# Optimization experiments

Hardware: AMD Instinct MI355X
Metric: run time of the kernel (lower is better)

## Reference

```python
import jax, jax.numpy as jnp
import numpy as np

# Config (matches init_kwargs)
HQ, HKV, HD, WIN = 16, 4, 128, 512  # query heads, kv heads, head_dim, sliding window


def setup_inputs() -> dict:
    key = jax.random.key(0)
    k0, k1, k2, k3, k4 = jax.random.split(key, 5)
    B, S, D = 1, 8192, 2048
    std = 0.02
    hidden_states = jax.random.normal(k0, (B, S, D), jnp.float32)
    Wq = jax.random.normal(k1, (D, HQ * HD), jnp.float32) * std
    Wk = jax.random.normal(k2, (D, HKV * HD), jnp.float32) * std
    Wv = jax.random.normal(k3, (D, HKV * HD), jnp.float32) * std
    Wo = jax.random.normal(k4, (HQ * HD, D), jnp.float32) * std
    return {"hidden_states": hidden_states, "Wq": Wq, "Wk": Wk, "Wv": Wv, "Wo": Wo}


def _sliding_window_attention(q, k, v, win):
    # block i attend to keys of blocks i-1 and i -> scores [B,H,nb,W,2W].
    B, H, S, hd = q.shape
    W = win
    nb = S // W
    qb = q.reshape(B, H, nb, W, hd)
    kpad = jnp.pad(k, ((0, 0), (0, 0), (W, 0), (0, 0)))
    vpad = jnp.pad(v, ((0, 0), (0, 0), (W, 0), (0, 0)))
    kb = jnp.concatenate([kpad[:, :, :S].reshape(B, H, nb, W, hd),
                          k.reshape(B, H, nb, W, hd)], axis=3)  # [B,H,nb,2W,hd]
    vb = jnp.concatenate([vpad[:, :, :S].reshape(B, H, nb, W, hd),
                          v.reshape(B, H, nb, W, hd)], axis=3)
    # Faithful double-scaling of the source: /sqrt(hd) inside the chunk matmul
    # and again before softmax -> effective /hd.
    scores = jnp.einsum('bhnqd,bhnkd->bhnqk', qb, kb) / jnp.asarray(hd, qb.dtype)
    qi = jnp.arange(W)[:, None]
    ki = jnp.arange(2 * W)[None, :]
    # key local index k maps to global offset (k - W) relative to block start;
    # attend iff 0 <= q_glob - k_glob <= W-1  <=>  q+1 <= k <= q+W
    band = (ki >= qi + 1) & (ki <= qi + W)          # [W, 2W]
    blk = jnp.arange(nb)[:, None, None]
    valid = band[None] & ((blk > 0) | (ki[None] >= W))  # block 0 has no prev keys
    neg = jnp.finfo(scores.dtype).min
    scores = jnp.where(valid[None, None], scores, neg)
    probs = jax.nn.softmax(scores, axis=-1)
    out = jnp.einsum('bhnqk,bhnkd->bhnqd', probs, vb)
    return out.reshape(B, H, S, hd)


def reference(hidden_states, Wq, Wk, Wv, Wo):
    B, S, D = hidden_states.shape
    q = (hidden_states @ Wq).reshape(B, S, HQ, HD).transpose(0, 2, 1, 3)
    k = (hidden_states @ Wk).reshape(B, S, HKV, HD).transpose(0, 2, 1, 3)
    v = (hidden_states @ Wv).reshape(B, S, HKV, HD).transpose(0, 2, 1, 3)
    rep = HQ // HKV
    k = jnp.repeat(k, rep, axis=1)
    v = jnp.repeat(v, rep, axis=1)
    attn = _sliding_window_attention(q, k, v, WIN)      # [B,HQ,S,HD]
    attn = attn.transpose(0, 2, 1, 3).reshape(B, S, HQ * HD)
    return attn @ Wo
```

## Files before the change

kernel.cpp:

```cpp
#include <hip/hip_runtime.h>


typedef __bf16 bf16x8 __attribute__((ext_vector_type(8)));
typedef float f32x4 __attribute__((ext_vector_type(4)));
typedef int v8i __attribute__((ext_vector_type(8)));

__device__ __forceinline__ unsigned short f2bf(float f) {
  unsigned int u = __float_as_uint(f);
  u += 0x7fffu + ((u >> 16) & 1u);
  return (unsigned short)(u >> 16);
}

__device__ __forceinline__ f32x4 mfma16(bf16x8 a, bf16x8 b, f32x4 c) {
  return __builtin_amdgcn_mfma_f32_16x16x32_bf16(a, b, c, 0, 0, 0);
}

__device__ __forceinline__ void async16(void* lds, const void* g) {
  __builtin_amdgcn_global_load_lds(
      (__attribute__((address_space(1))) unsigned int*)g,
      (__attribute__((address_space(3))) unsigned int*)lds, 16, 0, 0);
}


__global__ __launch_bounds__(256) void convert_h_kernel(
    const float* __restrict__ src, unsigned short* __restrict__ dbf,
    unsigned char* __restrict__ d8, int n) {
  int i = (blockIdx.x * 256 + threadIdx.x) * 4;
  if (i < n) {
    float4 f = *(const float4*)(src + i);
    ushort4 o;
    o.x = f2bf(f.x); o.y = f2bf(f.y); o.z = f2bf(f.z); o.w = f2bf(f.w);
    *(ushort4*)(dbf + i) = o;
    int p = __builtin_amdgcn_cvt_pk_fp8_f32(f.x, f.y, 0, 0);
    p = __builtin_amdgcn_cvt_pk_fp8_f32(f.z, f.w, p, 1);
    *(unsigned int*)(d8 + i) = p;
  }
}

__global__ __launch_bounds__(256) void transpose_convert_kernel(
    const float* __restrict__ src, unsigned short* __restrict__ dst,
    int K, int N) {
  __shared__ unsigned short T[64 * 72];
  int kb = blockIdx.y * 64, nb = blockIdx.x * 64;
  int t = threadIdx.x;
  for (int u = t; u < 1024; u += 256) {
    int r = u >> 4, s = u & 15;
    float4 f = *(const float4*)(src + (size_t)(kb + r) * N + nb + s * 4);
    ushort4 o;
    o.x = f2bf(f.x); o.y = f2bf(f.y); o.z = f2bf(f.z); o.w = f2bf(f.w);
    *(ushort4*)&T[r * 72 + s * 4] = o;
  }
  __syncthreads();
  for (int u = t; u < 1024; u += 256) {
    int orow = u >> 4, s = u & 15;
    ushort4 o;
    o.x = T[(s * 4 + 0) * 72 + orow];
    o.y = T[(s * 4 + 1) * 72 + orow];
    o.z = T[(s * 4 + 2) * 72 + orow];
    o.w = T[(s * 4 + 3) * 72 + orow];
    *(ushort4*)(dst + (size_t)(nb + orow) * K + kb + s * 4) = o;
  }
}

__global__ __launch_bounds__(256) void transpose_convert_fp8_kernel(
    const float* __restrict__ src, unsigned char* __restrict__ dst,
    int K, int N) {
  __shared__ unsigned short T[64 * 72];
  int kb = blockIdx.y * 64, nb = blockIdx.x * 64;
  int t = threadIdx.x;
  for (int u = t; u < 1024; u += 256) {
    int r = u >> 4, s = u & 15;
    float4 f = *(const float4*)(src + (size_t)(kb + r) * N + nb + s * 4);
    ushort4 o;
    o.x = f2bf(f.x); o.y = f2bf(f.y); o.z = f2bf(f.z); o.w = f2bf(f.w);
    *(ushort4*)&T[r * 72 + s * 4] = o;
  }
  __syncthreads();
  for (int u = t; u < 1024; u += 256) {
    int orow = u >> 4, s = u & 15;
    float f0 = __uint_as_float((unsigned int)T[(s * 4 + 0) * 72 + orow] << 16);
    float f1 = __uint_as_float((unsigned int)T[(s * 4 + 1) * 72 + orow] << 16);
    float f2 = __uint_as_float((unsigned int)T[(s * 4 + 2) * 72 + orow] << 16);
    float f3 = __uint_as_float((unsigned int)T[(s * 4 + 3) * 72 + orow] << 16);
    int p = __builtin_amdgcn_cvt_pk_fp8_f32(f0, f1, 0, 0);
    p = __builtin_amdgcn_cvt_pk_fp8_f32(f2, f3, p, 1);
    *(unsigned int*)&dst[(size_t)(nb + orow) * K + kb + s * 4] = p;
  }
}

__global__ __launch_bounds__(256) void vtrans_kernel(
    const unsigned short* __restrict__ QKV, unsigned short* __restrict__ VTg) {
  int flat = blockIdx.x * 256 + threadIdx.x;
  int c = flat & 511;
  int s0 = (flat >> 9) * 8;
  unsigned short tmp[8];
  #pragma unroll
  for (int j = 0; j < 8; ++j)
    tmp[j] = QKV[(size_t)(s0 + j) * 3072 + 2560 + c];
  *(uint4*)&VTg[(size_t)c * 8192 + s0] = *(uint4*)tmp;
}


template <bool F32OUT>
__global__ __launch_bounds__(256) void gemm_bt_kernel(
    const unsigned short* __restrict__ A, const unsigned short* __restrict__ BT,
    void* __restrict__ Cp, int M, int ldc, int K) {
  __shared__ unsigned short As[128 * 32];
  __shared__ unsigned short Bs[128 * 32];
  int mb = blockIdx.y * 128, nb = blockIdx.x * 128;
  int tid = threadIdx.x;
  int lane = tid & 63, wv = tid >> 6;
  int wrow = wv >> 1, wcol = wv & 1;
  int lr = lane >> 2, ls = lane & 3;
  int fr = lane & 15, fg = lane >> 4;
  f32x4 acc[4][4] = {};
  for (int k0 = 0; k0 < K; k0 += 32) {
    __syncthreads();
    #pragma unroll
    for (int r = 0; r < 2; ++r) {
      int s = wv * 2 + r;
      async16(&As[s * 512], &A[(size_t)(mb + s * 16 + lr) * K + k0 + ls * 8]);
      async16(&Bs[s * 512], &BT[(size_t)(nb + s * 16 + lr) * K + k0 + ls * 8]);
    }
    __syncthreads();
    bf16x8 a[4], b[4];
    #pragma unroll
    for (int rt = 0; rt < 4; ++rt)
      a[rt] = *(const bf16x8*)&As[(wrow * 64 + rt * 16 + fr) * 32 + fg * 8];
    #pragma unroll
    for (int ct = 0; ct < 4; ++ct)
      b[ct] = *(const bf16x8*)&Bs[(wcol * 64 + ct * 16 + fr) * 32 + fg * 8];
    #pragma unroll
    for (int rt = 0; rt < 4; ++rt)
      #pragma unroll
      for (int ct = 0; ct < 4; ++ct)
        acc[rt][ct] = mfma16(a[rt], b[ct], acc[rt][ct]);
  }
  #pragma unroll
  for (int rt = 0; rt < 4; ++rt)
    #pragma unroll
    for (int ct = 0; ct < 4; ++ct)
      #pragma unroll
      for (int i = 0; i < 4; ++i) {
        int row = mb + wrow * 64 + rt * 16 + fg * 4 + i;
        int col = nb + wcol * 64 + ct * 16 + fr;
        if constexpr (F32OUT)
          ((float*)Cp)[(size_t)row * ldc + col] = acc[rt][ct][i];
        else
          ((unsigned short*)Cp)[(size_t)row * ldc + col] = f2bf(acc[rt][ct][i]);
      }
}


__global__ __launch_bounds__(512, 2) void gemm8p_oproj_kernel(
    const unsigned short* __restrict__ A, const unsigned short* __restrict__ BT,
    float* __restrict__ C, int ldc, int K) {
  __shared__ unsigned char lds[131072];
  const int mb = blockIdx.y * 256, nb = blockIdx.x * 256;
  const int tid = threadIdx.x;
  const int lane = tid & 63, wv = tid >> 6;
  const int wm = wv >> 2, wn = wv & 3;
  const int fr = lane & 15, fg = lane >> 4;
  const int xr = (fr & 4) ? 32 : 0;
  const int a_base = (wm * 128 + fr) * 128 + ((fg * 16) ^ xr);
  const int b_base = (wn * 64 + fr) * 128 + ((fg * 16) ^ xr);
  const int lsw = (lane * 16) ^ (lane & 32);
  const int lrow = lsw >> 7, lcol = (lsw & 127) >> 1;
  const int NT = K >> 6;

  f32x4 acc[8][4] = {};
  bf16x8 aF[4][2], bF[2][2];

#define FENCE_ asm volatile("" ::: "memory")
#define BAR_ { FENCE_; __builtin_amdgcn_s_barrier(); FENCE_; }
#define LGKM0_ asm volatile("s_waitcnt lgkmcnt(0)" ::: "memory")
#define STAGE_A_(BUFI, T, HALF)                                              \
  { _Pragma("unroll")                                                        \
    for (int l = 0; l < 2; ++l) {                                            \
      int cc = wv * 2 + l;                                                   \
      int rb = (cc >> 3) * 128 + (HALF) * 64 + (cc & 7) * 8;                 \
      async16(lds + (BUFI) * 65536 + rb * 128,                               \
              A + (size_t)(mb + rb + lrow) * K + (T) * 64 + lcol);           \
    } }
#define STAGE_B_(BUFI, T, HALF)                                              \
  { _Pragma("unroll")                                                        \
    for (int l = 0; l < 2; ++l) {                                            \
      int cc = wv * 2 + l;                                                   \
      int rb = (cc >> 2) * 64 + (HALF) * 32 + (cc & 3) * 8;                  \
      async16(lds + (BUFI) * 65536 + 32768 + rb * 128,                       \
              BT + (size_t)(nb + rb + lrow) * K + (T) * 64 + lcol);          \
    } }
#define LOAD_A_(HALF)                                                        \
  { _Pragma("unroll")                                                        \
    for (int q = 0; q < 4; ++q)                                              \
      _Pragma("unroll")                                                      \
      for (int kk = 0; kk < 2; ++kk)                                         \
        aF[q][kk] =                                                          \
            *(const bf16x8*)&Ab_[a_base + ((HALF)*4 + q) * 2048 + kk * 64]; }
#define LOAD_B_(HALF)                                                        \
  { _Pragma("unroll")                                                        \
    for (int c2 = 0; c2 < 2; ++c2)                                           \
      _Pragma("unroll")                                                      \
      for (int kk = 0; kk < 2; ++kk)                                         \
        bF[c2][kk] =                                                         \
            *(const bf16x8*)&Bb_[b_base + ((HALF)*2 + c2) * 2048 + kk * 64]; }
#define MFMA_(RT0, CT0)                                                      \
  { __builtin_amdgcn_s_setprio(1);                                           \
    _Pragma("unroll")                                                        \
    for (int q = 0; q < 4; ++q)                                              \
      _Pragma("unroll")                                                      \
      for (int c2 = 0; c2 < 2; ++c2) {                                       \
        acc[(RT0) + q][(CT0) + c2] =                                         \
            mfma16(aF[q][0], bF[c2][0], acc[(RT0) + q][(CT0) + c2]);         \
        acc[(RT0) + q][(CT0) + c2] =                                         \
            mfma16(aF[q][1], bF[c2][1], acc[(RT0) + q][(CT0) + c2]);         \
      }                                                                      \
    __builtin_amdgcn_s_setprio(0); }

  STAGE_A_(0, 0, 0); STAGE_A_(0, 0, 1); STAGE_B_(0, 0, 0); STAGE_B_(0, 0, 1);
  STAGE_B_(1, 1, 0); STAGE_A_(1, 1, 1);
  asm volatile("s_waitcnt vmcnt(4)" ::: "memory");
  BAR_;

  for (int t = 0; t < NT; ++t) {
    const int cur = t & 1, nxt = cur ^ 1;
    const unsigned char* Ab_ = lds + cur * 65536;
    const unsigned char* Bb_ = Ab_ + 32768;
    LOAD_A_(0); LOAD_B_(0);
    if (t + 1 < NT) STAGE_A_(nxt, t + 1, 0);
    BAR_; LGKM0_;
    MFMA_(0, 0);
    BAR_;
    LOAD_A_(1);
    if (t + 1 < NT) STAGE_B_(nxt, t + 1, 1);
    BAR_; LGKM0_;
    MFMA_(4, 0);
    BAR_;
    LOAD_B_(1);
    if (t + 2 < NT) STAGE_B_(cur, t + 2, 0);
    BAR_; LGKM0_;
    MFMA_(4, 2);
    BAR_;
    LOAD_A_(0);
    if (t + 2 < NT) STAGE_A_(cur, t + 2, 1);
    BAR_; LGKM0_;
    MFMA_(0, 2);
    asm volatile("s_waitcnt vmcnt(4)" ::: "memory");
    BAR_;
  }

  #pragma unroll
  for (int rt = 0; rt < 8; ++rt)
    #pragma unroll
    for (int ct = 0; ct < 4; ++ct)
      #pragma unroll
      for (int i = 0; i < 4; ++i) {
        int row = mb + wm * 128 + rt * 16 + fg * 4 + i;
        int col = nb + wn * 64 + ct * 16 + fr;
        C[(size_t)row * ldc + col] = acc[rt][ct][i];
      }
#undef FENCE_
#undef BAR_
#undef LGKM0_
#undef STAGE_A_
#undef STAGE_B_
#undef LOAD_A_
#undef LOAD_B_
#undef MFMA_
}


__global__ __launch_bounds__(256) void gemm_qk_fp8_kernel(
    const unsigned char* __restrict__ A8, const unsigned char* __restrict__ B8,
    unsigned short* __restrict__ C, int M, int ldc, int K) {
  __shared__ unsigned char As[128 * 144];
  __shared__ unsigned char Bs[128 * 144];
  int mb = blockIdx.y * 128, nb = blockIdx.x * 128;
  int tid = threadIdx.x;
  int lane = tid & 63, wv = tid >> 6;
  int wrow = wv >> 1, wcol = wv & 1;
  int fr = lane & 15, fg = lane >> 4;
  int srow = tid >> 1, shalf = (tid & 1) * 64;
  f32x4 acc[4][4] = {};
  for (int k0 = 0; k0 < K; k0 += 128) {
    __syncthreads();
    #pragma unroll
    for (int j = 0; j < 4; ++j) {
      *(uint4*)&As[srow * 144 + shalf + j * 16] =
          *(const uint4*)&A8[(size_t)(mb + srow) * K + k0 + shalf + j * 16];
      *(uint4*)&Bs[srow * 144 + shalf + j * 16] =
          *(const uint4*)&B8[(size_t)(nb + srow) * K + k0 + shalf + j * 16];
    }
    __syncthreads();
    v8i a[4], b[4];
    #pragma unroll
    for (int rt = 0; rt < 4; ++rt) {
      int off = (wrow * 64 + rt * 16 + fr) * 144 + fg * 32;
      ((uint4*)&a[rt])[0] = *(const uint4*)&As[off];
      ((uint4*)&a[rt])[1] = *(const uint4*)&As[off + 16];
    }
    #pragma unroll
    for (int ct = 0; ct < 4; ++ct) {
      int off = (wcol * 64 + ct * 16 + fr) * 144 + fg * 32;
      ((uint4*)&b[ct])[0] = *(const uint4*)&Bs[off];
      ((uint4*)&b[ct])[1] = *(const uint4*)&Bs[off + 16];
    }
    #pragma unroll
    for (int rt = 0; rt < 4; ++rt)
      #pragma unroll
      for (int ct = 0; ct < 4; ++ct)
        acc[rt][ct] = __builtin_amdgcn_mfma_scale_f32_16x16x128_f8f6f4(
            a[rt], b[ct], acc[rt][ct], 0, 0,
            0, 0x7F7F7F7F,
            0, 0x7F7F7F7F);
  }
  #pragma unroll
  for (int rt = 0; rt < 4; ++rt)
    #pragma unroll
    for (int ct = 0; ct < 4; ++ct)
      #pragma unroll
      for (int i = 0; i < 4; ++i) {
        int row = mb + wrow * 64 + rt * 16 + fg * 4 + i;
        int col = nb + wcol * 64 + ct * 16 + fr;
        C[(size_t)row * ldc + col] = f2bf(acc[rt][ct][i]);
      }
}


#define SCALE_L2E 0.0112710027f

__global__ __launch_bounds__(512, 2) void attn_kernel(
    const unsigned short* __restrict__ QKV,
    const unsigned short* __restrict__ VTg,
    unsigned short* __restrict__ O) {
  __shared__ unsigned short Ks[64 * 136];
  __shared__ unsigned short VTs[128 * 72];
  __shared__ unsigned short Ps[8 * 32 * 72];
  const int g = blockIdx.y;
  const int qs = blockIdx.x * 64;
  const int tid = threadIdx.x;
  const int lane = tid & 63, w = tid >> 6;
  const int fr = lane & 15, fg = lane >> 4;
  const int hl = w & 3, qh = w >> 2;
  const int h = g * 4 + hl;
  const int kcol = 2048 + g * 128;
  unsigned short* Pw = &Ps[w * 32 * 72];

  bf16x8 qf[2][4];
  #pragma unroll
  for (int qt = 0; qt < 2; ++qt) {
    int qrow = qs + qh * 32 + qt * 16 + fr;
    #pragma unroll
    for (int kk = 0; kk < 4; ++kk)
      qf[qt][kk] = *(const bf16x8*)&QKV[(size_t)qrow * 3072 + h * 128 + kk * 32 + fg * 8];
  }
  f32x4 o_acc[2][8] = {};
  float l_part[2][4] = {};
  const int kb0 = qs >= 512 ? qs - 512 : 0;
  for (int kb = kb0; kb <= qs; kb += 64) {
    __syncthreads();
    #pragma unroll
    for (int it = 0; it < 2; ++it) {
      int u = tid + it * 512;
      int key = u >> 4, seg = u & 15;
      *(uint4*)&Ks[key * 136 + seg * 8] =
          *(const uint4*)&QKV[(size_t)(kb + key) * 3072 + kcol + seg * 8];
    }
    #pragma unroll
    for (int it = 0; it < 2; ++it) {
      int u = tid + it * 512;
      int d = u >> 3, seg = u & 7;
      *(uint4*)&VTs[d * 72 + seg * 8] =
          *(const uint4*)&VTg[(size_t)(g * 128 + d) * 8192 + kb + seg * 8];
    }
    __syncthreads();
    f32x4 s_acc[2][4] = {};
    #pragma unroll
    for (int kt = 0; kt < 4; ++kt) {
      bf16x8 kf[4];
      #pragma unroll
      for (int kk = 0; kk < 4; ++kk)
        kf[kk] = *(const bf16x8*)&Ks[(kt * 16 + fr) * 136 + kk * 32 + fg * 8];
      #pragma unroll
      for (int qt = 0; qt < 2; ++qt)
        #pragma unroll
        for (int kk = 0; kk < 4; ++kk)
          s_acc[qt][kt] = mfma16(qf[qt][kk], kf[kk], s_acc[qt][kt]);
    }
    const bool edge = (kb > qs - 64) || (kb < qs - 448);
    #pragma unroll
    for (int qt = 0; qt < 2; ++qt)
      #pragma unroll
      for (int kt = 0; kt < 4; ++kt)
        #pragma unroll
        for (int i = 0; i < 4; ++i) {
          float p = exp2f(s_acc[qt][kt][i] * SCALE_L2E);
          if (edge) {
            int kg = kb + kt * 16 + fr;
            int qg = qs + qh * 32 + qt * 16 + fg * 4 + i;
            if (kg > qg || kg < qg - 511) p = 0.f;
          }
          l_part[qt][i] += p;
          Pw[(qt * 16 + fg * 4 + i) * 72 + kt * 16 + fr] = f2bf(p);
        }
    bf16x8 af[2][2];
    #pragma unroll
    for (int qt = 0; qt < 2; ++qt)
      #pragma unroll
      for (int kf2 = 0; kf2 < 2; ++kf2)
        af[qt][kf2] = *(const bf16x8*)&Pw[(qt * 16 + fr) * 72 + kf2 * 32 + fg * 8];
    #pragma unroll
    for (int dt = 0; dt < 8; ++dt) {
      bf16x8 vf[2];
      #pragma unroll
      for (int kf2 = 0; kf2 < 2; ++kf2)
        vf[kf2] = *(const bf16x8*)&VTs[(dt * 16 + fr) * 72 + kf2 * 32 + fg * 8];
      #pragma unroll
      for (int qt = 0; qt < 2; ++qt)
        #pragma unroll
        for (int kf2 = 0; kf2 < 2; ++kf2)
          o_acc[qt][dt] = mfma16(af[qt][kf2], vf[kf2], o_acc[qt][dt]);
    }
  }
  #pragma unroll
  for (int qt = 0; qt < 2; ++qt)
    #pragma unroll
    for (int i = 0; i < 4; ++i) {
      float s = l_part[qt][i];
      s += __shfl_xor(s, 1); s += __shfl_xor(s, 2);
      s += __shfl_xor(s, 4); s += __shfl_xor(s, 8);
      l_part[qt][i] = 1.f / s;
    }
  #pragma unroll
  for (int qt = 0; qt < 2; ++qt)
    #pragma unroll
    for (int dt = 0; dt < 8; ++dt)
      #pragma unroll
      for (int i = 0; i < 4; ++i) {
        int row = qs + qh * 32 + qt * 16 + fg * 4 + i;
        O[(size_t)row * 2048 + h * 128 + dt * 16 + fr] =
            f2bf(o_acc[qt][dt][i] * l_part[qt][i]);
      }
}


extern "C" void kernel_launch(void* const* d_in, const int* in_sizes, int n_in,
                              void* d_out, int out_size, void* d_ws, size_t ws_size,
                              hipStream_t stream) {
  const float* h  = (const float*)d_in[0];
  const float* Wq = (const float*)d_in[1];
  const float* Wk = (const float*)d_in[2];
  const float* Wv = (const float*)d_in[3];
  const float* Wo = (const float*)d_in[4];
  float* out = (float*)d_out;
  char* ws = (char*)d_ws;
  const int S = 8192, D = 2048;
  const size_t MB = 1024 * 1024;

  unsigned short* QKV = (unsigned short*)(ws);
  unsigned short* hbf = (unsigned short*)(ws + 48 * MB);
  unsigned short* Ab  = hbf;
  unsigned char*  h8  = (unsigned char*)(ws + 80 * MB);
  unsigned short* VTg = (unsigned short*)(ws + 80 * MB);
  unsigned short* WoT = (unsigned short*)(ws + 88 * MB);
  unsigned char*  W8  = (unsigned char*)(ws + 96 * MB);
  unsigned short* WvT = (unsigned short*)(ws + 96 * MB);

  convert_h_kernel<<<16384, 256, 0, stream>>>(h, hbf, h8, S * D);
  transpose_convert_fp8_kernel<<<dim3(32, 32), 256, 0, stream>>>(Wq, W8, D, 2048);
  transpose_convert_fp8_kernel<<<dim3(8, 32), 256, 0, stream>>>(
      Wk, W8 + (size_t)2048 * 2048, D, 512);
  gemm_qk_fp8_kernel<<<dim3(20, 64), 256, 0, stream>>>(h8, W8, QKV, S, 3072, D);

  transpose_convert_kernel<<<dim3(8, 32), 256, 0, stream>>>(Wv, WvT, D, 512);
  gemm_bt_kernel<false><<<dim3(4, 64), 256, 0, stream>>>(hbf, WvT, QKV + 2560, S, 3072, D);

  vtrans_kernel<<<2048, 256, 0, stream>>>(QKV, VTg);
  transpose_convert_kernel<<<dim3(32, 32), 256, 0, stream>>>(Wo, WoT, D, 2048);
  attn_kernel<<<dim3(128, 4), 512, 0, stream>>>(QKV, VTg, Ab);
  gemm8p_oproj_kernel<<<dim3(8, 32), 512, 0, stream>>>(Ab, WoT, out, 2048, 2048);
}
```

Measured before the change: 429.4 us.

## Rewrite attention kernel with 32x32 MFMA, register-resident P, and prefetched K/V tiles

The attention kernel switches from 16x16x32 to 32x32x16 bf16 MFMA and computes S transposed (K as the A operand), so each lane owns one query row. P no longer goes through LDS: it is packed with v_cvt_pk_bf16_f32 and rearranged with v_permlane32_swap to form the A operand of the PV MFMA. The next K/V tile is loaded into registers during compute, which overlaps global loads with math but adds register pressure. It also sets s_setprio around the MFMA blocks, and the final normalization uses a small LDS buffer to redistribute row sums.

```diff
diff --git a/kernel.cpp b/kernel.cpp
--- a/kernel.cpp
+++ b/kernel.cpp
@@ -3,7 +3,9 @@
 
 typedef __bf16 bf16x8 __attribute__((ext_vector_type(8)));
 typedef float f32x4 __attribute__((ext_vector_type(4)));
+typedef float f32x16 __attribute__((ext_vector_type(16)));
 typedef int v8i __attribute__((ext_vector_type(8)));
+typedef unsigned int u32x4 __attribute__((ext_vector_type(4)));
 
 __device__ __forceinline__ unsigned short f2bf(float f) {
   unsigned int u = __float_as_uint(f);
@@ -13,6 +15,16 @@
 
 __device__ __forceinline__ f32x4 mfma16(bf16x8 a, bf16x8 b, f32x4 c) {
   return __builtin_amdgcn_mfma_f32_16x16x32_bf16(a, b, c, 0, 0, 0);
+}
+
+__device__ __forceinline__ f32x16 mfma32(bf16x8 a, bf16x8 b, f32x16 c) {
+  return __builtin_amdgcn_mfma_f32_32x32x16_bf16(a, b, c, 0, 0, 0);
+}
+
+__device__ __forceinline__ unsigned int cvtpk_bf16(float lo, float hi) {
+  unsigned int r;
+  asm volatile("v_cvt_pk_bf16_f32 %0, %1, %2" : "=v"(r) : "v"(lo), "v"(hi));
+  return r;
 }
 
 __device__ __forceinline__ void async16(void* lds, const void* g) {
@@ -335,112 +347,142 @@
     unsigned short* __restrict__ O) {
   __shared__ unsigned short Ks[64 * 136];
   __shared__ unsigned short VTs[128 * 72];
-  __shared__ unsigned short Ps[8 * 32 * 72];
+  __shared__ float Ls[8 * 32];
   const int g = blockIdx.y;
   const int qs = blockIdx.x * 64;
   const int tid = threadIdx.x;
   const int lane = tid & 63, w = tid >> 6;
-  const int fr = lane & 15, fg = lane >> 4;
+  const int l31 = lane & 31, hl2 = lane >> 5;
   const int hl = w & 3, qh = w >> 2;
   const int h = g * 4 + hl;
   const int kcol = 2048 + g * 128;
-  unsigned short* Pw = &Ps[w * 32 * 72];
-
-  bf16x8 qf[2][4];
+  const int qg = qs + qh * 32 + l31;
+
+  bf16x8 qf[8];
+  {
+    const unsigned short* qrow = &QKV[(size_t)qg * 3072 + h * 128];
+    #pragma unroll
+    for (int kk = 0; kk < 8; ++kk)
+      qf[kk] = *(const bf16x8*)&qrow[kk * 16 + hl2 * 8];
+  }
+
+  f32x16 o32[4] = {};
+  float l_lane = 0.f;
+
+  const int skey = tid >> 4, sseg = tid & 15;
+  const int sd = tid >> 3, sseg2 = tid & 7;
+
+  const int kb0 = qs >= 512 ? qs - 512 : 0;
+
+  {
+    uint4 kst[2], vst[2];
+    #pragma unroll
+    for (int it = 0; it < 2; ++it) {
+      kst[it] = *(const uint4*)&QKV[(size_t)(kb0 + skey + it * 32) * 3072 + kcol + sseg * 8];
+      vst[it] = *(const uint4*)&VTg[(size_t)(g * 128 + sd + it * 64) * 8192 + kb0 + sseg2 * 8];
+    }
+    #pragma unroll
+    for (int it = 0; it < 2; ++it) {
+      *(uint4*)&Ks[(skey + it * 32) * 136 + sseg * 8] = kst[it];
+      *(uint4*)&VTs[(sd + it * 64) * 72 + sseg2 * 8] = vst[it];
+    }
+  }
+  __syncthreads();
+
+  for (int kb = kb0; kb <= qs; kb += 64) {
+    const bool hasnext = (kb + 64 <= qs);
+    uint4 kn[2], vn[2];
+    if (hasnext) {
+      #pragma unroll
+      for (int it = 0; it < 2; ++it) {
+        kn[it] = *(const uint4*)&QKV[(size_t)(kb + 64 + skey + it * 32) * 3072 + kcol + sseg * 8];
+        vn[it] = *(const uint4*)&VTg[(size_t)(g * 128 + sd + it * 64) * 8192 + kb + 64 + sseg2 * 8];
+      }
+    }
+    f32x16 s32[2] = {};
+    __builtin_amdgcn_s_setprio(1);
+    #pragma unroll
+    for (int kt = 0; kt < 2; ++kt)
+      #pragma unroll
+      for (int kk = 0; kk < 8; ++kk) {
+        bf16x8 kf = *(const bf16x8*)&Ks[(kt * 32 + l31) * 136 + kk * 16 + hl2 * 8];
+        s32[kt] = mfma32(kf, qf[kk], s32[kt]);
+      }
+    __builtin_amdgcn_s_setprio(0);
+
+    const bool edge = (kb > qs - 64) || (kb < qs - 448);
+    unsigned int u[2][4][2];
+    #pragma unroll
+    for (int kt = 0; kt < 2; ++kt) {
+      float p[16];
+      #pragma unroll
+      for (int r = 0; r < 16; ++r) {
+        float pv = exp2f(s32[kt][r] * SCALE_L2E);
+        if (edge) {
+          int kg = kb + kt * 32 + (r & 3) + 8 * (r >> 2) + 4 * hl2;
+          if (kg > qg || kg < qg - 511) pv = 0.f;
+        }
+        l_lane += pv;
+        p[r] = pv;
+      }
+      #pragma unroll
+      for (int gr = 0; gr < 4; ++gr) {
+        u[kt][gr][0] = cvtpk_bf16(p[4 * gr + 0], p[4 * gr + 1]);
+        u[kt][gr][1] = cvtpk_bf16(p[4 * gr + 2], p[4 * gr + 3]);
+      }
+    }
+
+    bf16x8 af[4];
+    #pragma unroll
+    for (int kc = 0; kc < 4; ++kc) {
+      const int kt = kc >> 1;
+      const int gLo = 2 * (kc & 1), gHi = gLo + 1;
+      unsigned int xa0 = u[kt][gLo][0], xb0 = u[kt][gHi][0];
+      unsigned int xa1 = u[kt][gLo][1], xb1 = u[kt][gHi][1];
+      asm volatile("v_permlane32_swap_b32 %0, %1" : "+v"(xa0), "+v"(xb0));
+      asm volatile("v_permlane32_swap_b32 %0, %1" : "+v"(xa1), "+v"(xb1));
+      u32x4 t;
+      t[0] = xa0; t[1] = xa1; t[2] = xb0; t[3] = xb1;
+      af[kc] = __builtin_bit_cast(bf16x8, t);
+    }
+
+    __builtin_amdgcn_s_setprio(1);
+    #pragma unroll
+    for (int dc = 0; dc < 4; ++dc)
+      #pragma unroll
+      for (int kc = 0; kc < 4; ++kc) {
+        bf16x8 vf = *(const bf16x8*)&VTs[(dc * 32 + l31) * 72 + kc * 16 + hl2 * 8];
+        o32[dc] = mfma32(af[kc], vf, o32[dc]);
+      }
+    __builtin_amdgcn_s_setprio(0);
+
+    __syncthreads();
+    if (hasnext) {
+      #pragma unroll
+      for (int it = 0; it < 2; ++it) {
+        *(uint4*)&Ks[(skey + it * 32) * 136 + sseg * 8] = kn[it];
+        *(uint4*)&VTs[(sd + it * 64) * 72 + sseg2 * 8] = vn[it];
+      }
+      __syncthreads();
+    }
+  }
+
+  l_lane += __shfl_xor(l_lane, 32);
+  float linv = 1.f / l_lane;
+  Ls[w * 32 + l31] = linv;
+  asm volatile("s_waitcnt lgkmcnt(0)" ::: "memory");
+  float lr[16];
   #pragma unroll
-  for (int qt = 0; qt < 2; ++qt) {
-    int qrow = qs + qh * 32 + qt * 16 + fr;
-    #pragma unroll
-    for (int kk = 0; kk < 4; ++kk)
-      qf[qt][kk] = *(const bf16x8*)&QKV[(size_t)qrow * 3072 + h * 128 + kk * 32 + fg * 8];
-  }
-  f32x4 o_acc[2][8] = {};
-  float l_part[2][4] = {};
-  const int kb0 = qs >= 512 ? qs - 512 : 0;
-  for (int kb = kb0; kb <= qs; kb += 64) {
-    __syncthreads();
-    #pragma unroll
-    for (int it = 0; it < 2; ++it) {
-      int u = tid + it * 512;
-      int key = u >> 4, seg = u & 15;
-      *(uint4*)&Ks[key * 136 + seg * 8] =
-          *(const uint4*)&QKV[(size_t)(kb + key) * 3072 + kcol + seg * 8];
-    }
-    #pragma unroll
-    for (int it = 0; it < 2; ++it) {
-      int u = tid + it * 512;
-      int d = u >> 3, seg = u & 7;
-      *(uint4*)&VTs[d * 72 + seg * 8] =
-          *(const uint4*)&VTg[(size_t)(g * 128 + d) * 8192 + kb + seg * 8];
-    }
-    __syncthreads();
-    f32x4 s_acc[2][4] = {};
-    #pragma unroll
-    for (int kt = 0; kt < 4; ++kt) {
-      bf16x8 kf[4];
-      #pragma unroll
-      for (int kk = 0; kk < 4; ++kk)
-        kf[kk] = *(const bf16x8*)&Ks[(kt * 16 + fr) * 136 + kk * 32 + fg * 8];
-      #pragma unroll
-      for (int qt = 0; qt < 2; ++qt)
-        #pragma unroll
-        for (int kk = 0; kk < 4; ++kk)
-          s_acc[qt][kt] = mfma16(qf[qt][kk], kf[kk], s_acc[qt][kt]);
-    }
-    const bool edge = (kb > qs - 64) || (kb < qs - 448);
-    #pragma unroll
-    for (int qt = 0; qt < 2; ++qt)
-      #pragma unroll
-      for (int kt = 0; kt < 4; ++kt)
-        #pragma unroll
-        for (int i = 0; i < 4; ++i) {
-          float p = exp2f(s_acc[qt][kt][i] * SCALE_L2E);
-          if (edge) {
-            int kg = kb + kt * 16 + fr;
-            int qg = qs + qh * 32 + qt * 16 + fg * 4 + i;
-            if (kg > qg || kg < qg - 511) p = 0.f;
-          }
-          l_part[qt][i] += p;
-          Pw[(qt * 16 + fg * 4 + i) * 72 + kt * 16 + fr] = f2bf(p);
-        }
-    bf16x8 af[2][2];
-    #pragma unroll
-    for (int qt = 0; qt < 2; ++qt)
-      #pragma unroll
-      for (int kf2 = 0; kf2 < 2; ++kf2)
-        af[qt][kf2] = *(const bf16x8*)&Pw[(qt * 16 + fr) * 72 + kf2 * 32 + fg * 8];
-    #pragma unroll
-    for (int dt = 0; dt < 8; ++dt) {
-      bf16x8 vf[2];
-      #pragma unroll
-      for (int kf2 = 0; kf2 < 2; ++kf2)
-        vf[kf2] = *(const bf16x8*)&VTs[(dt * 16 + fr) * 72 + kf2 * 32 + fg * 8];
-      #pragma unroll
-      for (int qt = 0; qt < 2; ++qt)
-        #pragma unroll
-        for (int kf2 = 0; kf2 < 2; ++kf2)
-          o_acc[qt][dt] = mfma16(af[qt][kf2], vf[kf2], o_acc[qt][dt]);
-    }
-  }
+  for (int r = 0; r < 16; ++r)
+    lr[r] = Ls[w * 32 + (r & 3) + 8 * (r >> 2) + 4 * hl2];
   #pragma unroll
-  for (int qt = 0; qt < 2; ++qt)
-    #pragma unroll
-    for (int i = 0; i < 4; ++i) {
-      float s = l_part[qt][i];
-      s += __shfl_xor(s, 1); s += __shfl_xor(s, 2);
-      s += __shfl_xor(s, 4); s += __shfl_xor(s, 8);
-      l_part[qt][i] = 1.f / s;
-    }
-  #pragma unroll
-  for (int qt = 0; qt < 2; ++qt)
-    #pragma unroll
-    for (int dt = 0; dt < 8; ++dt)
-      #pragma unroll
-      for (int i = 0; i < 4; ++i) {
-        int row = qs + qh * 32 + qt * 16 + fg * 4 + i;
-        O[(size_t)row * 2048 + h * 128 + dt * 16 + fr] =
-            f2bf(o_acc[qt][dt][i] * l_part[qt][i]);
-      }
+  for (int dc = 0; dc < 4; ++dc)
+    #pragma unroll
+    for (int r = 0; r < 16; ++r) {
+      int row = qs + qh * 32 + (r & 3) + 8 * (r >> 2) + 4 * hl2;
+      O[(size_t)row * 2048 + h * 128 + dc * 32 + l31] =
+          f2bf(o32[dc][r] * lr[r]);
+    }
 }
 
 
```

Result: slower. 446.3 us (+3.9%).
